# Optimization experiments

Measured on AMD Instinct MI355X. Metric: run time of the kernel, lower is better.

## Reference

```python
import jax, jax.numpy as jnp
import numpy as np

CLAMP = 1000000.0
LN_EPS = 1e-5


def setup_inputs() -> dict:
    key = jax.random.key(0)
    ks = jax.random.split(key, 4)
    Bsz, L, D, S = 4, 4096, 1024, 64
    x = jax.random.normal(ks[0], (Bsz, L, D), dtype=jnp.float32)
    A = jax.random.normal(ks[1], (S, S), dtype=jnp.float32) * 0.01
    Bm = jax.random.normal(ks[2], (S, D), dtype=jnp.float32) * 0.01
    C = jax.random.normal(ks[3], (D, S), dtype=jnp.float32) * 0.01
    gamma = jnp.ones((D,), dtype=jnp.float32)
    beta = jnp.zeros((D,), dtype=jnp.float32)
    return {"x": x, "A": A, "Bm": Bm, "C": C, "gamma": gamma, "beta": beta}


def _ssm_forward(x, A, Bm, C, gamma, beta):
    Bsz, L, D = x.shape
    S = A.shape[0]
    # Precompute input projection as one big GEMM: u_t @ B.T for all t -> [B, L, S]
    uB = jnp.einsum('bld,sd->bls', x, Bm)
    # Sequential linear recurrence: state_t = state_{t-1} @ A.T + uB_t
    def step(state, u_t):
        s = state @ A.T + u_t  # [B, S]
        return s, s
    init = jnp.zeros((Bsz, S), dtype=x.dtype)
    _, states = jax.lax.scan(step, init, jnp.swapaxes(uB, 0, 1))  # [L, B, S]
    states = jnp.swapaxes(states, 0, 1)  # [B, L, S]
    # Output projection as one big GEMM: y_t = state_t @ C.T
    y = jnp.einsum('bls,ds->bld', states, C)
    act = jax.nn.gelu(y, approximate=False)  # torch nn.GELU default = exact erf
    mean = jnp.mean(act, axis=-1, keepdims=True)
    var = jnp.mean(jnp.square(act - mean), axis=-1, keepdims=True)  # biased, like LayerNorm
    normed = (act - mean) * jax.lax.rsqrt(var + LN_EPS) * gamma + beta
    return jnp.nan_to_num(normed, nan=0.0, posinf=CLAMP, neginf=-CLAMP)


def reference(x, A, Bm, C, gamma, beta):
    return _ssm_forward(x, A, Bm, C, gamma, beta)
```

## Files before the change

### kernel.cpp

```cpp
#include <hip/hip_runtime.h>
#include <hip/hip_bf16.h>
#include <math.h>

#define Bsz  4
#define Lseq 4096
#define Dd   1024
#define Ss   64
#define RTOT (Bsz*Lseq)

#define LC   16
#define WARM 12
#define CHUNKS_PER_B (Lseq/LC)

typedef __attribute__((ext_vector_type(8))) short short8;
typedef __attribute__((ext_vector_type(4))) float f32x4;

__device__ __forceinline__ ushort f2bf(float f) {
  unsigned u = __float_as_uint(f);
  unsigned r = (u + 0x7FFFu + ((u >> 16) & 1u)) >> 16;
  return (ushort)r;
}

__device__ __forceinline__ unsigned cvtpk(float lo, float hi) {
  __hip_bfloat162 h = __float22bfloat162_rn(make_float2(lo, hi));
  union { __hip_bfloat162 h; unsigned u; } c; c.h = h;
  return c.u;
}

__device__ __forceinline__ short8 pack8v(f32x4 a, f32x4 b) {
  union { short8 s; unsigned u[4]; } r;
  r.u[0] = cvtpk(a[0], a[1]);
  r.u[1] = cvtpk(a[2], a[3]);
  r.u[2] = cvtpk(b[0], b[1]);
  r.u[3] = cvtpk(b[2], b[3]);
  return r.s;
}

__device__ __forceinline__ float gelu_erf(float v) {
  float x  = v * 0.70710678118654752f;
  float ax = fabsf(x);
  float t  = __builtin_amdgcn_rcpf(fmaf(0.3275911f, ax, 1.f));
  float p  = fmaf(1.061405429f, t, -1.453152027f);
  p = fmaf(p, t, 1.421413741f);
  p = fmaf(p, t, -0.284496736f);
  p = fmaf(p, t, 0.254829592f);
  p = p * t;
  float e  = __expf(-x * x);
  float er = fmaf(-p, e, 1.f);
  er = copysignf(er, x);
  return 0.5f * v * (1.f + er);
}

__global__ __launch_bounds__(256) void k_prep(const float* __restrict__ Bm,
                                              const float* __restrict__ C,
                                              ushort* __restrict__ Bmb,
                                              ushort* __restrict__ Cb) {
  int idx = blockIdx.x * 256 + threadIdx.x;
  const float* src; ushort* dst; int off;
  if (idx < 16384) { src = Bm; dst = Bmb; off = idx; }
  else             { src = C;  dst = Cb;  off = idx - 16384; }
  float4 v = *(const float4*)&src[(size_t)off*4];
  ushort4 o;
  o.x = f2bf(v.x); o.y = f2bf(v.y); o.z = f2bf(v.z); o.w = f2bf(v.w);
  *(ushort4*)&dst[(size_t)off*4] = o;
}

__global__ __launch_bounds__(256, 3) void k_gemm1(const float* __restrict__ x,
                                                  const ushort* __restrict__ Bmb,
                                                  float* __restrict__ uB) {
  const int l  = threadIdx.x & 63;
  const int wv = threadIdx.x >> 6;
  const int wm = wv >> 1, wn = wv & 1;
  const int row0 = blockIdx.x * 32 + wm * 16;
  const int n0   = wn * 32;
  const int lr = l & 15, lq = l >> 4;

  f32x4 acc0 = {0.f,0.f,0.f,0.f}, acc1 = {0.f,0.f,0.f,0.f};
  const f32x4*  xa  = (const f32x4*)(x + (size_t)(row0 + lr) * Dd + 8*lq);
  const ushort* bp0 = Bmb + (size_t)(n0      + lr) * Dd + 8*lq;
  const ushort* bp1 = Bmb + (size_t)(n0 + 16 + lr) * Dd + 8*lq;

  #pragma unroll 16
  for (int ks = 0; ks < 32; ++ks) {
    f32x4 alo = xa[8*ks];
    f32x4 ahi = xa[8*ks + 1];
    short8 b0 = *(const short8*)(bp0 + 32*ks);
    short8 b1 = *(const short8*)(bp1 + 32*ks);
    short8 a  = pack8v(alo, ahi);
    acc0 = __builtin_amdgcn_mfma_f32_16x16x32_bf16(a, b0, acc0, 0, 0, 0);
    acc1 = __builtin_amdgcn_mfma_f32_16x16x32_bf16(a, b1, acc1, 0, 0, 0);
  }
  const int orow = row0 + 4*lq;
  #pragma unroll
  for (int j = 0; j < 4; ++j) {
    uB[(size_t)(orow + j)*Ss + n0 + lr]      = acc0[j];
    uB[(size_t)(orow + j)*Ss + n0 + 16 + lr] = acc1[j];
  }
}

__device__ __forceinline__ float bcast_lane(float v, int l) {
  return __int_as_float(__builtin_amdgcn_readlane(__float_as_int(v), l));
}

__global__ __launch_bounds__(256) void k_scan(const float* __restrict__ uB,
                                              const float* __restrict__ A,
                                              ushort* __restrict__ stb) {
  const int lane  = threadIdx.x & 63;
  const int wv    = threadIdx.x >> 6;
  const int chunk = blockIdx.x * 4 + wv;
  const int b     = chunk >> 8;
  const int c     = chunk & (CHUNKS_PER_B-1);

  float arow[64];
  #pragma unroll
  for (int i = 0; i < 64; i += 4) {
    float4 v = *(const float4*)&A[lane*64 + i];
    arow[i] = v.x; arow[i+1] = v.y; arow[i+2] = v.z; arow[i+3] = v.w;
  }

  const int cs = c * LC;
  const int t0 = (cs >= WARM) ? (cs - WARM) : 0;
  float s = 0.f;
  const float* up = uB  + ((size_t)b*Lseq + t0)*Ss + lane;
  ushort*      sp = stb + ((size_t)b*Lseq + cs)*Ss + lane;

  for (int tt = t0; tt < cs + LC; ++tt, up += Ss) {
    float u = *up;
    float a0 = u, a1 = 0.f, a2 = 0.f, a3 = 0.f;
    #pragma unroll
    for (int i = 0; i < 64; i += 4) {
      a0 += bcast_lane(s, i  ) * arow[i  ];
      a1 += bcast_lane(s, i+1) * arow[i+1];
      a2 += bcast_lane(s, i+2) * arow[i+2];
      a3 += bcast_lane(s, i+3) * arow[i+3];
    }
    s = (a0 + a1) + (a2 + a3);
    if (tt >= cs) { *sp = f2bf(s); sp += Ss; }
  }
}

__device__ __forceinline__ float fixv(float v) {
  if (isnan(v)) return 0.f;
  if (isinf(v)) return v > 0.f ? 1000000.0f : -1000000.0f;
  return v;
}

__global__ __launch_bounds__(256, 2) void k_out(const ushort* __restrict__ stb,
                                                const ushort* __restrict__ Cb,
                                                const float* __restrict__ gamma,
                                                const float* __restrict__ beta,
                                                float* __restrict__ out) {
  __shared__ float reds[4][2][16];
  __shared__ float redq[4][2][16];
  __shared__ float mrs[32][2];
  const int t  = threadIdx.x;
  const int l  = t & 63;
  const int wv = t >> 6;
  const int lr = l & 15, lq = l >> 4;
  const size_t row0 = (size_t)blockIdx.x * 32;

  const ushort* sp0 = stb + (row0      + lr)*Ss + 8*lq;
  const ushort* sp1 = stb + (row0 + 16 + lr)*Ss + 8*lq;
  short8 sA0 = *(const short8*)(sp0);
  short8 sA1 = *(const short8*)(sp0 + 32);
  short8 sB0 = *(const short8*)(sp1);
  short8 sB1 = *(const short8*)(sp1 + 32);

  const int d0 = wv * 256;
  f32x4 accA[16], accB[16];
  #pragma unroll
  for (int tt = 0; tt < 16; ++tt) {
    accA[tt] = (f32x4){0.f,0.f,0.f,0.f};
    accB[tt] = (f32x4){0.f,0.f,0.f,0.f};
  }

  const ushort* cbase = Cb + (size_t)(d0 + lr)*Ss + 8*lq;
  #pragma unroll
  for (int tt = 0; tt < 16; ++tt) {
    const ushort* cp = cbase + (size_t)tt*16*Ss;
    short8 c0 = *(const short8*)(cp);
    short8 c1 = *(const short8*)(cp + 32);
    accA[tt] = __builtin_amdgcn_mfma_f32_16x16x32_bf16(c0, sA0, accA[tt], 0, 0, 0);
    accA[tt] = __builtin_amdgcn_mfma_f32_16x16x32_bf16(c1, sA1, accA[tt], 0, 0, 0);
    accB[tt] = __builtin_amdgcn_mfma_f32_16x16x32_bf16(c0, sB0, accB[tt], 0, 0, 0);
    accB[tt] = __builtin_amdgcn_mfma_f32_16x16x32_bf16(c1, sB1, accB[tt], 0, 0, 0);
  }

  float psA = 0.f, pqA = 0.f, psB = 0.f, pqB = 0.f;
  #pragma unroll
  for (int tt = 0; tt < 16; ++tt) {
    #pragma unroll
    for (int j = 0; j < 4; ++j) {
      float gA = gelu_erf(accA[tt][j]);
      accA[tt][j] = gA; psA += gA; pqA += gA * gA;
      float gB = gelu_erf(accB[tt][j]);
      accB[tt][j] = gB; psB += gB; pqB += gB * gB;
    }
  }
  psA += __shfl_xor(psA, 16); psA += __shfl_xor(psA, 32);
  pqA += __shfl_xor(pqA, 16); pqA += __shfl_xor(pqA, 32);
  psB += __shfl_xor(psB, 16); psB += __shfl_xor(psB, 32);
  pqB += __shfl_xor(pqB, 16); pqB += __shfl_xor(pqB, 32);
  if (l < 16) {
    reds[wv][0][l] = psA; redq[wv][0][l] = pqA;
    reds[wv][1][l] = psB; redq[wv][1][l] = pqB;
  }
  __syncthreads();
  if (t < 32) {
    const int rg = t >> 4, r = t & 15;
    float sm = reds[0][rg][r] + reds[1][rg][r] + reds[2][rg][r] + reds[3][rg][r];
    float sq = redq[0][rg][r] + redq[1][rg][r] + redq[2][rg][r] + redq[3][rg][r];
    float mean = sm * (1.f/1024.f);
    float var  = sq * (1.f/1024.f) - mean*mean;
    mrs[t][0] = mean;
    mrs[t][1] = rsqrtf(var + 1e-5f);
  }
  __syncthreads();

  const float meanA = mrs[lr][0],      rsigA = mrs[lr][1];
  const float meanB = mrs[16 + lr][0], rsigB = mrs[16 + lr][1];
  float* orowA = out + (row0      + lr)*Dd;
  float* orowB = out + (row0 + 16 + lr)*Dd;
  #pragma unroll
  for (int tt = 0; tt < 16; ++tt) {
    const int d = d0 + 16*tt + 4*lq;
    float4 g4 = *(const float4*)&gamma[d];
    float4 b4 = *(const float4*)&beta[d];
    f32x4 oA, oB;
    #pragma unroll
    for (int j = 0; j < 4; ++j) {
      float gj = (&g4.x)[j], bj = (&b4.x)[j];
      oA[j] = fixv(fmaf((accA[tt][j] - meanA) * rsigA, gj, bj));
      oB[j] = fixv(fmaf((accB[tt][j] - meanB) * rsigB, gj, bj));
    }
    *(f32x4*)&orowA[d] = oA;
    *(f32x4*)&orowB[d] = oB;
  }
}

extern "C" void kernel_launch(void* const* d_in, const int* in_sizes, int n_in,
                              void* d_out, int out_size, void* d_ws, size_t ws_size,
                              hipStream_t stream) {
  (void)in_sizes; (void)n_in; (void)out_size; (void)ws_size;
  const float* x     = (const float*)d_in[0];
  const float* A     = (const float*)d_in[1];
  const float* Bm    = (const float*)d_in[2];
  const float* C     = (const float*)d_in[3];
  const float* gamma = (const float*)d_in[4];
  const float* beta  = (const float*)d_in[5];
  float* out = (float*)d_out;

  float*  uB  = (float*)d_ws;
  ushort* stb = (ushort*)(uB + (size_t)RTOT * Ss);
  ushort* Cb  = stb + (size_t)RTOT * Ss;
  ushort* Bmb = Cb + (size_t)Dd * Ss;

  k_prep <<<128, 256, 0, stream>>>(Bm, C, Bmb, Cb);
  k_gemm1<<<RTOT/32, 256, 0, stream>>>(x, Bmb, uB);
  k_scan <<<(Bsz*CHUNKS_PER_B)/4, 256, 0, stream>>>(uB, A, stb);
  k_out  <<<RTOT/32, 256, 0, stream>>>(stb, Cb, gamma, beta, out);
}
```

Measured before the change: 84.61 us.

## Split-K input GEMM with register prefetch and double-buffer C loads in output kernel

The input projection kernel now gives each block 16 rows instead of 32 and splits the K dimension across wave pairs. The two partial sums are combined through shared memory, which doubles the grid. Each wave also prefetches four K-steps of x and B into registers to hide global load latency. The output kernel double-buffers its C-tile loads so the next tile is fetched while the current MFMAs run, at the cost of some extra registers and a block-wide barrier in gemm1.

Result: no change. 85.32 us (+0.8%).

```diff
diff --git a/kernel.cpp b/kernel.cpp
--- a/kernel.cpp
+++ b/kernel.cpp
@@ -65,36 +65,60 @@
   *(ushort4*)&dst[(size_t)off*4] = o;
 }
 
-__global__ __launch_bounds__(256, 3) void k_gemm1(const float* __restrict__ x,
-                                                  const ushort* __restrict__ Bmb,
-                                                  float* __restrict__ uB) {
+#define PF1 4
+__global__ __launch_bounds__(256) void k_gemm1(const float* __restrict__ x,
+                                               const ushort* __restrict__ Bmb,
+                                               float* __restrict__ uB) {
+  __shared__ float part[2][16][32];
   const int l  = threadIdx.x & 63;
-  const int wv = threadIdx.x >> 6;
-  const int wm = wv >> 1, wn = wv & 1;
-  const int row0 = blockIdx.x * 32 + wm * 16;
-  const int n0   = wn * 32;
+  const int w  = threadIdx.x >> 6;
+  const int kh = w >> 1, nh = w & 1;
+  const int row0 = blockIdx.x * 16;
+  const int n0   = nh * 32;
   const int lr = l & 15, lq = l >> 4;
 
+  const float*  xp  = x   + (size_t)(row0 + lr)*Dd + kh*512 + 8*lq;
+  const ushort* bp0 = Bmb + (size_t)(n0      + lr)*Dd + kh*512 + 8*lq;
+  const ushort* bp1 = Bmb + (size_t)(n0 + 16 + lr)*Dd + kh*512 + 8*lq;
+
+  f32x4  xl[PF1], xh[PF1];
+  short8 b0[PF1], b1[PF1];
+  #pragma unroll
+  for (int p = 0; p < PF1; ++p) {
+    xl[p] = *(const f32x4*)(xp + 32*p);
+    xh[p] = *(const f32x4*)(xp + 32*p + 4);
+    b0[p] = *(const short8*)(bp0 + 32*p);
+    b1[p] = *(const short8*)(bp1 + 32*p);
+  }
   f32x4 acc0 = {0.f,0.f,0.f,0.f}, acc1 = {0.f,0.f,0.f,0.f};
-  const f32x4*  xa  = (const f32x4*)(x + (size_t)(row0 + lr) * Dd + 8*lq);
-  const ushort* bp0 = Bmb + (size_t)(n0      + lr) * Dd + 8*lq;
-  const ushort* bp1 = Bmb + (size_t)(n0 + 16 + lr) * Dd + 8*lq;
-
-  #pragma unroll 16
-  for (int ks = 0; ks < 32; ++ks) {
-    f32x4 alo = xa[8*ks];
-    f32x4 ahi = xa[8*ks + 1];
-    short8 b0 = *(const short8*)(bp0 + 32*ks);
-    short8 b1 = *(const short8*)(bp1 + 32*ks);
-    short8 a  = pack8v(alo, ahi);
-    acc0 = __builtin_amdgcn_mfma_f32_16x16x32_bf16(a, b0, acc0, 0, 0, 0);
-    acc1 = __builtin_amdgcn_mfma_f32_16x16x32_bf16(a, b1, acc1, 0, 0, 0);
-  }
-  const int orow = row0 + 4*lq;
-  #pragma unroll
-  for (int j = 0; j < 4; ++j) {
-    uB[(size_t)(orow + j)*Ss + n0 + lr]      = acc0[j];
-    uB[(size_t)(orow + j)*Ss + n0 + 16 + lr] = acc1[j];
+  #pragma unroll
+  for (int ks = 0; ks < 16; ++ks) {
+    const int s = ks & (PF1-1);
+    short8 a = pack8v(xl[s], xh[s]);
+    acc0 = __builtin_amdgcn_mfma_f32_16x16x32_bf16(a, b0[s], acc0, 0, 0, 0);
+    acc1 = __builtin_amdgcn_mfma_f32_16x16x32_bf16(a, b1[s], acc1, 0, 0, 0);
+    if (ks + PF1 < 16) {
+      xl[s] = *(const f32x4*)(xp + 32*(ks+PF1));
+      xh[s] = *(const f32x4*)(xp + 32*(ks+PF1) + 4);
+      b0[s] = *(const short8*)(bp0 + 32*(ks+PF1));
+      b1[s] = *(const short8*)(bp1 + 32*(ks+PF1));
+    }
+  }
+  if (kh == 1) {
+    #pragma unroll
+    for (int j = 0; j < 4; ++j) {
+      part[nh][4*lq + j][lr]      = acc0[j];
+      part[nh][4*lq + j][16 + lr] = acc1[j];
+    }
+  }
+  __syncthreads();
+  if (kh == 0) {
+    const int orow = row0 + 4*lq;
+    #pragma unroll
+    for (int j = 0; j < 4; ++j) {
+      uB[(size_t)(orow + j)*Ss + n0 + lr]      = acc0[j] + part[nh][4*lq + j][lr];
+      uB[(size_t)(orow + j)*Ss + n0 + 16 + lr] = acc1[j] + part[nh][4*lq + j][16 + lr];
+    }
   }
 }
 
@@ -175,15 +199,21 @@
   }
 
   const ushort* cbase = Cb + (size_t)(d0 + lr)*Ss + 8*lq;
-  #pragma unroll
-  for (int tt = 0; tt < 16; ++tt) {
-    const ushort* cp = cbase + (size_t)tt*16*Ss;
-    short8 c0 = *(const short8*)(cp);
-    short8 c1 = *(const short8*)(cp + 32);
-    accA[tt] = __builtin_amdgcn_mfma_f32_16x16x32_bf16(c0, sA0, accA[tt], 0, 0, 0);
-    accA[tt] = __builtin_amdgcn_mfma_f32_16x16x32_bf16(c1, sA1, accA[tt], 0, 0, 0);
-    accB[tt] = __builtin_amdgcn_mfma_f32_16x16x32_bf16(c0, sB0, accB[tt], 0, 0, 0);
-    accB[tt] = __builtin_amdgcn_mfma_f32_16x16x32_bf16(c1, sB1, accB[tt], 0, 0, 0);
+  short8 c0[2], c1[2];
+  c0[0] = *(const short8*)(cbase);
+  c1[0] = *(const short8*)(cbase + 32);
+  #pragma unroll
+  for (int tt = 0; tt < 16; ++tt) {
+    const int s = tt & 1;
+    if (tt < 15) {
+      const ushort* cn = cbase + (size_t)(tt+1)*16*Ss;
+      c0[s^1] = *(const short8*)(cn);
+      c1[s^1] = *(const short8*)(cn + 32);
+    }
+    accA[tt] = __builtin_amdgcn_mfma_f32_16x16x32_bf16(c0[s], sA0, accA[tt], 0, 0, 0);
+    accA[tt] = __builtin_amdgcn_mfma_f32_16x16x32_bf16(c1[s], sA1, accA[tt], 0, 0, 0);
+    accB[tt] = __builtin_amdgcn_mfma_f32_16x16x32_bf16(c0[s], sB0, accB[tt], 0, 0, 0);
+    accB[tt] = __builtin_amdgcn_mfma_f32_16x16x32_bf16(c1[s], sB1, accB[tt], 0, 0, 0);
   }
 
   float psA = 0.f, pqA = 0.f, psB = 0.f, pqB = 0.f;
@@ -256,7 +286,7 @@
   ushort* Bmb = Cb + (size_t)Dd * Ss;
 
   k_prep <<<128, 256, 0, stream>>>(Bm, C, Bmb, Cb);
-  k_gemm1<<<RTOT/32, 256, 0, stream>>>(x, Bmb, uB);
+  k_gemm1<<<RTOT/16, 256, 0, stream>>>(x, Bmb, uB);
   k_scan <<<(Bsz*CHUNKS_PER_B)/4, 256, 0, stream>>>(uB, A, stb);
   k_out  <<<RTOT/32, 256, 0, stream>>>(stb, Cb, gamma, beta, out);
 }
```

## Split-K input projection with bf16 partials, finer scan chunks, wider output blocks

Applied to the files above, without the earlier changes.

The input GEMM is split along K into four partial products stored as bf16, so more blocks run in parallel. Summing the partials moves into the scan, which also halves its chunk length to 8 for more parallel chunks at the cost of more warm-up recompute. The output kernel now uses 512 threads with each wave covering 128 columns, which lowers per-thread register use. A fallback path with an in-block split-K GEMM is chosen when the workspace is too small; the bf16 partials add rounding error to the scan input.

Result: slower. 99.59 us (+17.7%).

```diff
diff --git a/kernel.cpp b/kernel.cpp
--- a/kernel.cpp
+++ b/kernel.cpp
@@ -8,9 +8,9 @@
 #define Ss   64
 #define RTOT (Bsz*Lseq)
 
-#define LC   16
-#define WARM 12
-#define CHUNKS_PER_B (Lseq/LC)
+#define LC8   8
+#define WARM  12
+#define LC16  16
 
 typedef __attribute__((ext_vector_type(8))) short short8;
 typedef __attribute__((ext_vector_type(4))) float f32x4;
@@ -20,13 +20,14 @@
   unsigned r = (u + 0x7FFFu + ((u >> 16) & 1u)) >> 16;
   return (ushort)r;
 }
-
+__device__ __forceinline__ float b2f(ushort v) {
+  return __uint_as_float(((unsigned)v) << 16);
+}
 __device__ __forceinline__ unsigned cvtpk(float lo, float hi) {
   __hip_bfloat162 h = __float22bfloat162_rn(make_float2(lo, hi));
   union { __hip_bfloat162 h; unsigned u; } c; c.h = h;
   return c.u;
 }
-
 __device__ __forceinline__ short8 pack8v(f32x4 a, f32x4 b) {
   union { short8 s; unsigned u[4]; } r;
   r.u[0] = cvtpk(a[0], a[1]);
@@ -51,6 +52,16 @@
   return 0.5f * v * (1.f + er);
 }
 
+__device__ __forceinline__ float fixv(float v) {
+  if (isnan(v)) return 0.f;
+  if (isinf(v)) return v > 0.f ? 1000000.0f : -1000000.0f;
+  return v;
+}
+
+__device__ __forceinline__ float bcast_lane(float v, int l) {
+  return __int_as_float(__builtin_amdgcn_readlane(__float_as_int(v), l));
+}
+
 __global__ __launch_bounds__(256) void k_prep(const float* __restrict__ Bm,
                                               const float* __restrict__ C,
                                               ushort* __restrict__ Bmb,
@@ -65,51 +76,125 @@
   *(ushort4*)&dst[(size_t)off*4] = o;
 }
 
-__global__ __launch_bounds__(256, 3) void k_gemm1(const float* __restrict__ x,
-                                                  const ushort* __restrict__ Bmb,
-                                                  float* __restrict__ uB) {
+__global__ __launch_bounds__(256) void k_gemm1s(const float* __restrict__ x,
+                                                const ushort* __restrict__ Bmb,
+                                                ushort* __restrict__ part) {
   const int l  = threadIdx.x & 63;
-  const int wv = threadIdx.x >> 6;
-  const int wm = wv >> 1, wn = wv & 1;
-  const int row0 = blockIdx.x * 32 + wm * 16;
-  const int n0   = wn * 32;
+  const int w  = threadIdx.x >> 6;
+  const int rt = blockIdx.x >> 2, kq = blockIdx.x & 3;
+  const int row0 = rt * 16, n0 = w * 16;
   const int lr = l & 15, lq = l >> 4;
 
+  const float*  xp = x   + (size_t)(row0 + lr)*Dd + kq*256 + 8*lq;
+  const ushort* bp = Bmb + (size_t)(n0   + lr)*Dd + kq*256 + 8*lq;
+
+  f32x4 acc = {0.f,0.f,0.f,0.f};
+  #pragma unroll
+  for (int ks = 0; ks < 8; ++ks) {
+    f32x4 alo = *(const f32x4*)(xp + 32*ks);
+    f32x4 ahi = *(const f32x4*)(xp + 32*ks + 4);
+    short8 b  = *(const short8*)(bp + 32*ks);
+    short8 a  = pack8v(alo, ahi);
+    acc = __builtin_amdgcn_mfma_f32_16x16x32_bf16(a, b, acc, 0, 0, 0);
+  }
+  ushort* pp = part + (size_t)kq * RTOT * Ss;
+  const int orow = row0 + 4*lq;
+  #pragma unroll
+  for (int j = 0; j < 4; ++j)
+    pp[(size_t)(orow + j)*Ss + n0 + lr] = f2bf(acc[j]);
+}
+
+__global__ __launch_bounds__(256) void k_scans(const ushort* __restrict__ part,
+                                               const float* __restrict__ A,
+                                               ushort* __restrict__ stb) {
+  const int lane  = threadIdx.x & 63;
+  const int wv    = threadIdx.x >> 6;
+  const int chunk = blockIdx.x * 4 + wv;
+  const int b     = chunk >> 9;
+  const int c     = chunk & 511;
+
+  float arow[64];
+  #pragma unroll
+  for (int i = 0; i < 64; i += 4) {
+    float4 v = *(const float4*)&A[lane*64 + i];
+    arow[i] = v.x; arow[i+1] = v.y; arow[i+2] = v.z; arow[i+3] = v.w;
+  }
+
+  const int cs = c * LC8;
+  const int t0 = (cs >= WARM) ? (cs - WARM) : 0;
+  const size_t KQ = (size_t)RTOT * Ss;
+  float s = 0.f;
+  const ushort* up = part + ((size_t)b*Lseq + t0)*Ss + lane;
+  ushort*       sp = stb  + ((size_t)b*Lseq + cs)*Ss + lane;
+
+  for (int tt = t0; tt < cs + LC8; ++tt, up += Ss) {
+    float u = (b2f(up[0]) + b2f(up[KQ])) + (b2f(up[2*KQ]) + b2f(up[3*KQ]));
+    float a0 = u, a1 = 0.f, a2 = 0.f, a3 = 0.f;
+    #pragma unroll
+    for (int i = 0; i < 64; i += 4) {
+      a0 += bcast_lane(s, i  ) * arow[i  ];
+      a1 += bcast_lane(s, i+1) * arow[i+1];
+      a2 += bcast_lane(s, i+2) * arow[i+2];
+      a3 += bcast_lane(s, i+3) * arow[i+3];
+    }
+    s = (a0 + a1) + (a2 + a3);
+    if (tt >= cs) { *sp = f2bf(s); sp += Ss; }
+  }
+}
+
+#define PF1 4
+__global__ __launch_bounds__(256) void k_gemm1o(const float* __restrict__ x,
+                                                const ushort* __restrict__ Bmb,
+                                                float* __restrict__ uB) {
+  __shared__ float partl[2][16][32];
+  const int l  = threadIdx.x & 63;
+  const int w  = threadIdx.x >> 6;
+  const int kh = w >> 1, nh = w & 1;
+  const int row0 = blockIdx.x * 16;
+  const int n0   = nh * 32;
+  const int lr = l & 15, lq = l >> 4;
+
+  const float*  xp  = x   + (size_t)(row0 + lr)*Dd + kh*512 + 8*lq;
+  const ushort* bp0 = Bmb + (size_t)(n0      + lr)*Dd + kh*512 + 8*lq;
+  const ushort* bp1 = Bmb + (size_t)(n0 + 16 + lr)*Dd + kh*512 + 8*lq;
+
   f32x4 acc0 = {0.f,0.f,0.f,0.f}, acc1 = {0.f,0.f,0.f,0.f};
-  const f32x4*  xa  = (const f32x4*)(x + (size_t)(row0 + lr) * Dd + 8*lq);
-  const ushort* bp0 = Bmb + (size_t)(n0      + lr) * Dd + 8*lq;
-  const ushort* bp1 = Bmb + (size_t)(n0 + 16 + lr) * Dd + 8*lq;
-
-  #pragma unroll 16
-  for (int ks = 0; ks < 32; ++ks) {
-    f32x4 alo = xa[8*ks];
-    f32x4 ahi = xa[8*ks + 1];
+  #pragma unroll
+  for (int ks = 0; ks < 16; ++ks) {
+    f32x4 alo = *(const f32x4*)(xp + 32*ks);
+    f32x4 ahi = *(const f32x4*)(xp + 32*ks + 4);
     short8 b0 = *(const short8*)(bp0 + 32*ks);
     short8 b1 = *(const short8*)(bp1 + 32*ks);
     short8 a  = pack8v(alo, ahi);
     acc0 = __builtin_amdgcn_mfma_f32_16x16x32_bf16(a, b0, acc0, 0, 0, 0);
     acc1 = __builtin_amdgcn_mfma_f32_16x16x32_bf16(a, b1, acc1, 0, 0, 0);
   }
-  const int orow = row0 + 4*lq;
-  #pragma unroll
-  for (int j = 0; j < 4; ++j) {
-    uB[(size_t)(orow + j)*Ss + n0 + lr]      = acc0[j];
-    uB[(size_t)(orow + j)*Ss + n0 + 16 + lr] = acc1[j];
-  }
-}
-
-__device__ __forceinline__ float bcast_lane(float v, int l) {
-  return __int_as_float(__builtin_amdgcn_readlane(__float_as_int(v), l));
-}
-
-__global__ __launch_bounds__(256) void k_scan(const float* __restrict__ uB,
-                                              const float* __restrict__ A,
-                                              ushort* __restrict__ stb) {
+  if (kh == 1) {
+    #pragma unroll
+    for (int j = 0; j < 4; ++j) {
+      partl[nh][4*lq + j][lr]      = acc0[j];
+      partl[nh][4*lq + j][16 + lr] = acc1[j];
+    }
+  }
+  __syncthreads();
+  if (kh == 0) {
+    const int orow = row0 + 4*lq;
+    #pragma unroll
+    for (int j = 0; j < 4; ++j) {
+      uB[(size_t)(orow + j)*Ss + n0 + lr]      = acc0[j] + partl[nh][4*lq + j][lr];
+      uB[(size_t)(orow + j)*Ss + n0 + 16 + lr] = acc1[j] + partl[nh][4*lq + j][16 + lr];
+    }
+  }
+}
+
+__global__ __launch_bounds__(256) void k_scano(const float* __restrict__ uB,
+                                               const float* __restrict__ A,
+                                               ushort* __restrict__ stb) {
   const int lane  = threadIdx.x & 63;
   const int wv    = threadIdx.x >> 6;
   const int chunk = blockIdx.x * 4 + wv;
   const int b     = chunk >> 8;
-  const int c     = chunk & (CHUNKS_PER_B-1);
+  const int c     = chunk & 255;
 
   float arow[64];
   #pragma unroll
@@ -117,14 +202,12 @@
     float4 v = *(const float4*)&A[lane*64 + i];
     arow[i] = v.x; arow[i+1] = v.y; arow[i+2] = v.z; arow[i+3] = v.w;
   }
-
-  const int cs = c * LC;
+  const int cs = c * LC16;
   const int t0 = (cs >= WARM) ? (cs - WARM) : 0;
   float s = 0.f;
   const float* up = uB  + ((size_t)b*Lseq + t0)*Ss + lane;
   ushort*      sp = stb + ((size_t)b*Lseq + cs)*Ss + lane;
-
-  for (int tt = t0; tt < cs + LC; ++tt, up += Ss) {
+  for (int tt = t0; tt < cs + LC16; ++tt, up += Ss) {
     float u = *up;
     float a0 = u, a1 = 0.f, a2 = 0.f, a3 = 0.f;
     #pragma unroll
@@ -139,19 +222,13 @@
   }
 }
 
-__device__ __forceinline__ float fixv(float v) {
-  if (isnan(v)) return 0.f;
-  if (isinf(v)) return v > 0.f ? 1000000.0f : -1000000.0f;
-  return v;
-}
-
-__global__ __launch_bounds__(256, 2) void k_out(const ushort* __restrict__ stb,
+__global__ __launch_bounds__(512, 4) void k_out(const ushort* __restrict__ stb,
                                                 const ushort* __restrict__ Cb,
                                                 const float* __restrict__ gamma,
                                                 const float* __restrict__ beta,
                                                 float* __restrict__ out) {
-  __shared__ float reds[4][2][16];
-  __shared__ float redq[4][2][16];
+  __shared__ float reds[8][2][16];
+  __shared__ float redq[8][2][16];
   __shared__ float mrs[32][2];
   const int t  = threadIdx.x;
   const int l  = t & 63;
@@ -166,17 +243,17 @@
   short8 sB0 = *(const short8*)(sp1);
   short8 sB1 = *(const short8*)(sp1 + 32);
 
-  const int d0 = wv * 256;
-  f32x4 accA[16], accB[16];
-  #pragma unroll
-  for (int tt = 0; tt < 16; ++tt) {
+  const int d0 = wv * 128;
+  f32x4 accA[8], accB[8];
+  #pragma unroll
+  for (int tt = 0; tt < 8; ++tt) {
     accA[tt] = (f32x4){0.f,0.f,0.f,0.f};
     accB[tt] = (f32x4){0.f,0.f,0.f,0.f};
   }
 
   const ushort* cbase = Cb + (size_t)(d0 + lr)*Ss + 8*lq;
   #pragma unroll
-  for (int tt = 0; tt < 16; ++tt) {
+  for (int tt = 0; tt < 8; ++tt) {
     const ushort* cp = cbase + (size_t)tt*16*Ss;
     short8 c0 = *(const short8*)(cp);
     short8 c1 = *(const short8*)(cp + 32);
@@ -188,7 +265,7 @@
 
   float psA = 0.f, pqA = 0.f, psB = 0.f, pqB = 0.f;
   #pragma unroll
-  for (int tt = 0; tt < 16; ++tt) {
+  for (int tt = 0; tt < 8; ++tt) {
     #pragma unroll
     for (int j = 0; j < 4; ++j) {
       float gA = gelu_erf(accA[tt][j]);
@@ -208,8 +285,9 @@
   __syncthreads();
   if (t < 32) {
     const int rg = t >> 4, r = t & 15;
-    float sm = reds[0][rg][r] + reds[1][rg][r] + reds[2][rg][r] + reds[3][rg][r];
-    float sq = redq[0][rg][r] + redq[1][rg][r] + redq[2][rg][r] + redq[3][rg][r];
+    float sm = 0.f, sq = 0.f;
+    #pragma unroll
+    for (int w = 0; w < 8; ++w) { sm += reds[w][rg][r]; sq += redq[w][rg][r]; }
     float mean = sm * (1.f/1024.f);
     float var  = sq * (1.f/1024.f) - mean*mean;
     mrs[t][0] = mean;
@@ -222,7 +300,7 @@
   float* orowA = out + (row0      + lr)*Dd;
   float* orowB = out + (row0 + 16 + lr)*Dd;
   #pragma unroll
-  for (int tt = 0; tt < 16; ++tt) {
+  for (int tt = 0; tt < 8; ++tt) {
     const int d = d0 + 16*tt + 4*lq;
     float4 g4 = *(const float4*)&gamma[d];
     float4 b4 = *(const float4*)&beta[d];
@@ -241,7 +319,7 @@
 extern "C" void kernel_launch(void* const* d_in, const int* in_sizes, int n_in,
                               void* d_out, int out_size, void* d_ws, size_t ws_size,
                               hipStream_t stream) {
-  (void)in_sizes; (void)n_in; (void)out_size; (void)ws_size;
+  (void)in_sizes; (void)n_in; (void)out_size;
   const float* x     = (const float*)d_in[0];
   const float* A     = (const float*)d_in[1];
   const float* Bm    = (const float*)d_in[2];
@@ -250,13 +328,26 @@
   const float* beta  = (const float*)d_in[5];
   float* out = (float*)d_out;
 
-  float*  uB  = (float*)d_ws;
-  ushort* stb = (ushort*)(uB + (size_t)RTOT * Ss);
-  ushort* Cb  = stb + (size_t)RTOT * Ss;
-  ushort* Bmb = Cb + (size_t)Dd * Ss;
-
-  k_prep <<<128, 256, 0, stream>>>(Bm, C, Bmb, Cb);
-  k_gemm1<<<RTOT/32, 256, 0, stream>>>(x, Bmb, uB);
-  k_scan <<<(Bsz*CHUNKS_PER_B)/4, 256, 0, stream>>>(uB, A, stb);
-  k_out  <<<RTOT/32, 256, 0, stream>>>(stb, Cb, gamma, beta, out);
-}
+  const size_t NP = (size_t)RTOT * Ss;
+  const size_t needNew = 4*NP*2 + NP*2 + 2*(size_t)Dd*Ss*2;
+
+  if (ws_size >= needNew) {
+    ushort* part = (ushort*)d_ws;
+    ushort* stb  = part + 4*NP;
+    ushort* Cb   = stb + NP;
+    ushort* Bmb  = Cb + (size_t)Dd * Ss;
+    k_prep  <<<128, 256, 0, stream>>>(Bm, C, Bmb, Cb);
+    k_gemm1s<<<(RTOT/16)*4, 256, 0, stream>>>(x, Bmb, part);
+    k_scans <<<(Bsz*(Lseq/LC8))/4, 256, 0, stream>>>(part, A, stb);
+    k_out   <<<RTOT/32, 512, 0, stream>>>(stb, Cb, gamma, beta, out);
+  } else {
+    float*  uB  = (float*)d_ws;
+    ushort* stb = (ushort*)(uB + NP);
+    ushort* Cb  = stb + NP;
+    ushort* Bmb = Cb + (size_t)Dd * Ss;
+    k_prep  <<<128, 256, 0, stream>>>(Bm, C, Bmb, Cb);
+    k_gemm1o<<<RTOT/16, 256, 0, stream>>>(x, Bmb, uB);
+    k_scano <<<(Bsz*(Lseq/LC16))/4, 256, 0, stream>>>(uB, A, stb);
+    k_out   <<<RTOT/32, 512, 0, stream>>>(stb, Cb, gamma, beta, out);
+  }
+}
```
